# Optimization experiments

Measured on AMD Instinct MI355X. Metric: run time of the kernel, lower is better.

## Reference

```python
import jax, jax.numpy as jnp
import numpy as np


def reference(x, coef_ref, coef_qry):
    # x: [B, Hr, Wr, Hq, Wq] similarity tensor
    B, Hr, Wr, Hq, Wq = x.shape
    xr = x.reshape(B, Hr * Wr, Hq * Wq)  # [B, R, Q]
    # softmax over ref axis (axis=1) of coef_ref * (x - max over axis 1)
    xm_ref = xr - jnp.max(xr, axis=1, keepdims=True)
    conf_ref = jax.nn.softmax(coef_ref[0] * xm_ref, axis=1)
    # softmax over qry axis (axis=2) of coef_qry * (x - max over axis 2)
    xm_qry = xr - jnp.max(xr, axis=2, keepdims=True)
    conf_qry = jax.nn.softmax(coef_qry[0] * xm_qry, axis=2)
    confidence = jnp.sqrt(conf_ref * conf_qry)  # [B, R, Q]
    # top_k(k=1) over last axis + gather_nd of that value == max over axis 2
    values = jnp.max(confidence, axis=2)  # [B, R]
    return values.reshape(B, Hr, Wr, 1)


def setup_inputs() -> dict:
    key = jax.random.key(0)
    k1, = jax.random.split(key, 1)
    B, Hr, Wr, Hq, Wq = 16, 64, 64, 32, 32
    alpha = 10.0
    x = jax.random.normal(k1, (B, Hr, Wr, Hq, Wq), dtype=jnp.float32)
    coef_ref = jnp.full((1,), alpha, dtype=jnp.float32)
    coef_qry = jnp.full((1,), alpha, dtype=jnp.float32)
    return {"x": x, "coef_ref": coef_ref, "coef_qry": coef_qry}
```

## Files before the change

### kernel.cpp

```cpp
#include <hip/hip_runtime.h>
#include <math.h>
#include <stdint.h>


constexpr int B = 16;
constexpr int R = 4096;
constexpr int Q = 1024;
constexpr int CAP = 32;
constexpr int CHROWS = 16;
constexpr int NCH = R / CHROWS;
constexpr int NBLK = B * NCH;
#define DTH 1.1f
#define ECLAMP 80.f

__device__ __forceinline__ float wmax64(float v) {
#pragma unroll
    for (int o = 32; o; o >>= 1) v = fmaxf(v, __shfl_xor(v, o, 64));
    return v;
}
__device__ __forceinline__ float max4(float4 v) {
    return fmaxf(fmaxf(v.x, v.y), fmaxf(v.z, v.w));
}
__device__ __forceinline__ uint32_t encf(float f) {
    uint32_t u = __float_as_uint(f);
    return (u & 0x80000000u) ? ~u : (u | 0x80000000u);
}
__device__ __forceinline__ float decf(uint32_t e) {
    uint32_t u = (e & 0x80000000u) ? (e & 0x7FFFFFFFu) : ~e;
    return __uint_as_float(u);
}

__global__ __launch_bounds__(256, 8) void qatm_pass1(
    const float* __restrict__ x,
    float* __restrict__ psum,
    float2* __restrict__ rscnt,
    float4* __restrict__ cand4,
    uint32_t* __restrict__ candg,
    float* __restrict__ thChunk,
    uint32_t* __restrict__ cminEnc,
    const float* __restrict__ coef_ref,
    const float* __restrict__ coef_qry)
{
    const int blk = blockIdx.x;
    const int b = blk >> 8, ch = blk & (NCH - 1);
    const int t = threadIdx.x;
    const float ar = coef_ref[0], aq = coef_qry[0];
    const bool same = (ar == aq);

    __shared__ float ssum[CHROWS][257];
    __shared__ int cnt_sh[CHROWS];
    __shared__ float redsh[4];
    __shared__ float th_sh;

    if (blk < B && t == 0) cminEnc[blk] = 0xFFFFFFFFu;

    const size_t row0 = (size_t)b * R + (size_t)ch * CHROWS;
    const float4* xb = reinterpret_cast<const float4*>(x) + row0 * 256 + t;

    if (t < CHROWS) cnt_sh[t] = 0;
    {
        float m = wmax64(max4(xb[0]));
        if ((t & 63) == 0) redsh[t >> 6] = m;
        __syncthreads();
        if (t == 0) {
            float mm = fmaxf(fmaxf(redsh[0], redsh[1]), fmaxf(redsh[2], redsh[3]));
            th_sh = mm - DTH;
            thChunk[blk] = mm - DTH;
        }
        __syncthreads();
    }
    const float th = th_sh;

    float4 c = {0.f, 0.f, 0.f, 0.f};

#pragma unroll 4
    for (int r = 0; r < CHROWS; ++r) {
        float4 v = xb[(size_t)r * 256];
        float4 e;
        e.x = __expf(fminf(ar * v.x, ECLAMP));
        e.y = __expf(fminf(ar * v.y, ECLAMP));
        e.z = __expf(fminf(ar * v.z, ECLAMP));
        e.w = __expf(fminf(ar * v.w, ECLAMP));
        c.x += e.x; c.y += e.y; c.z += e.z; c.w += e.w;
        float rp;
        if (same) rp = (e.x + e.y) + (e.z + e.w);
        else rp = (__expf(fminf(aq * v.x, ECLAMP)) + __expf(fminf(aq * v.y, ECLAMP))) +
                  (__expf(fminf(aq * v.z, ECLAMP)) + __expf(fminf(aq * v.w, ECLAMP)));
        ssum[r][t] = rp;
        if (max4(v) >= th) {
            int idx = atomicAdd(&cnt_sh[r], 1);
            if (idx < CAP) {
                cand4[(row0 + r) * CAP + idx] = v;
                candg[(row0 + r) * CAP + idx] = (uint32_t)t;
            }
        }
    }

    __syncthreads();
    {
        const int row = t >> 4, seg = t & 15;
        float p = 0.f;
#pragma unroll
        for (int i = 0; i < 16; ++i) p += ssum[row][seg + 16 * i];
        p += __shfl_xor(p, 1, 64);
        p += __shfl_xor(p, 2, 64);
        p += __shfl_xor(p, 4, 64);
        p += __shfl_xor(p, 8, 64);
        if (seg == 0)
            rscnt[row0 + row] = make_float2(p, __uint_as_float((uint32_t)cnt_sh[row]));
    }
    reinterpret_cast<float4*>(psum)[(size_t)blk * 256 + t] = c;
}

__global__ __launch_bounds__(256) void qatm_combine(
    const float* __restrict__ psum, float* __restrict__ cvec,
    uint32_t* __restrict__ cminEnc)
{
    const int b = blockIdx.x >> 4, part = blockIdx.x & 15;
    const int t = threadIdx.x;
    const int col = part * 64 + (t & 63);
    const int stripe = t >> 6;
    __shared__ float acc[4][64];
    float s = 0.f;
    const float* p = psum + ((size_t)b * NCH + (size_t)stripe * 64) * 1024 + col;
#pragma unroll 8
    for (int i = 0; i < 64; ++i) s += p[(size_t)i * 1024];
    acc[stripe][t & 63] = s;
    __syncthreads();
    if (t < 64) {
        float tot = (acc[0][t] + acc[1][t]) + (acc[2][t] + acc[3][t]);
        float c = __logf(tot);
        cvec[b * 1024 + col] = c;
        float m = -wmax64(-c);
        if (t == 0) atomicMin(&cminEnc[b], encf(m));
    }
}

__global__ __launch_bounds__(256) void qatm_select(
    const float* __restrict__ x, const float* __restrict__ cvec,
    const uint32_t* __restrict__ cminEnc, const float* __restrict__ thChunk,
    const float2* __restrict__ rscnt,
    const float4* __restrict__ cand4, const uint32_t* __restrict__ candg,
    const float* __restrict__ coef_ref, const float* __restrict__ coef_qry,
    float* __restrict__ out)
{
    const int w = threadIdx.x >> 6, l = threadIdx.x & 63;
    const size_t row = (size_t)blockIdx.x * 4 + w;
    const int b = (int)(row >> 12);
    const float ar = coef_ref[0], aq = coef_qry[0], s2 = ar + aq;
    const float2 rc = rscnt[row];
    const float rs = rc.x;
    const uint32_t cnt = __float_as_uint(rc.y);

    float best = -INFINITY;
    bool fb = (cnt > CAP) || (cnt == 0) || !(s2 > 0.f);
    if (!fb) {
        if (l < (int)cnt) {
            float4 v = cand4[row * CAP + l];
            uint32_t g = candg[row * CAP + l];
            float4 c = reinterpret_cast<const float4*>(cvec)[((size_t)b << 8) + (int)(g & 255u)];
            best = fmaxf(fmaxf(s2 * v.x - c.x, s2 * v.y - c.y),
                         fmaxf(s2 * v.z - c.z, s2 * v.w - c.w));
        }
        best = wmax64(best);
        if (!(best >= s2 * thChunk[row >> 4] - decf(cminEnc[b]))) fb = true;
    }
    if (fb) {
        const float4* xr = reinterpret_cast<const float4*>(x) + row * (Q / 4);
        const float4* cq = reinterpret_cast<const float4*>(cvec) + ((size_t)b << 8);
        best = -INFINITY;
#pragma unroll
        for (int it = 0; it < 4; ++it) {
            float4 v = xr[it * 64 + l], c = cq[it * 64 + l];
            best = fmaxf(best, fmaxf(fmaxf(s2 * v.x - c.x, s2 * v.y - c.y),
                                     fmaxf(s2 * v.z - c.z, s2 * v.w - c.w)));
        }
        best = wmax64(best);
    }
    if (l == 0) out[row] = __expf(0.5f * (best - __logf(rs)));
}

extern "C" void kernel_launch(void* const* d_in, const int* in_sizes, int n_in,
                              void* d_out, int out_size, void* d_ws, size_t ws_size,
                              hipStream_t stream) {
    const float* x = (const float*)d_in[0];
    const float* coef_ref = (const float*)d_in[1];
    const float* coef_qry = (const float*)d_in[2];
    float* out = (float*)d_out;

    char* ws = (char*)d_ws;
    size_t off = 0;
    float4*   cand4 = (float4*)(ws + off);   off += (size_t)B * R * CAP * 16;
    uint32_t* candg = (uint32_t*)(ws + off); off += (size_t)B * R * CAP * 4;
    float*    psum  = (float*)(ws + off);    off += (size_t)NBLK * 1024 * 4;
    float*    cvec  = (float*)(ws + off);    off += (size_t)B * Q * 4;
    float2*   rscnt = (float2*)(ws + off);   off += (size_t)B * R * 8;
    float*    thA   = (float*)(ws + off);    off += (size_t)NBLK * 4;
    uint32_t* cminE = (uint32_t*)(ws + off); off += 64;

    qatm_pass1<<<NBLK, 256, 0, stream>>>(x, psum, rscnt, cand4, candg,
                                         thA, cminE, coef_ref, coef_qry);
    qatm_combine<<<256, 256, 0, stream>>>(psum, cvec, cminE);
    qatm_select<<<(B * R) / 4, 256, 0, stream>>>(x, cvec, cminE, thA, rscnt,
                                                 cand4, candg, coef_ref, coef_qry, out);
}
```

Baseline: 85.01 us.

## Store per-element candidates compactly in shared memory and batch select rows

Candidates are now recorded per scalar element as (value, column index) pairs, buffered in shared memory and written out coalesced at the end of the block, replacing scattered global writes of float4 plus group index. The main loop loads four rows at once with nontemporal loads to raise memory-level parallelism and avoid polluting cache. The select kernel handles four rows per wave, and the candidate cap drops to 16 elements, which shrinks workspace traffic. The cost is a higher chance of overflowing the cap and taking the full-row fallback, plus a serial atomic loop over set bits.

```diff
diff --git a/kernel.cpp b/kernel.cpp
--- a/kernel.cpp
+++ b/kernel.cpp
@@ -6,20 +6,19 @@
 constexpr int B = 16;
 constexpr int R = 4096;
 constexpr int Q = 1024;
-constexpr int CAP = 32;
+constexpr int CAPE = 16;
 constexpr int CHROWS = 16;
 constexpr int NCH = R / CHROWS;
 constexpr int NBLK = B * NCH;
 #define DTH 1.1f
 #define ECLAMP 80.f
 
+typedef float float4n __attribute__((ext_vector_type(4)));
+
 __device__ __forceinline__ float wmax64(float v) {
 #pragma unroll
     for (int o = 32; o; o >>= 1) v = fmaxf(v, __shfl_xor(v, o, 64));
     return v;
-}
-__device__ __forceinline__ float max4(float4 v) {
-    return fmaxf(fmaxf(v.x, v.y), fmaxf(v.z, v.w));
 }
 __device__ __forceinline__ uint32_t encf(float f) {
     uint32_t u = __float_as_uint(f);
@@ -34,8 +33,7 @@
     const float* __restrict__ x,
     float* __restrict__ psum,
     float2* __restrict__ rscnt,
-    float4* __restrict__ cand4,
-    uint32_t* __restrict__ candg,
+    float2* __restrict__ cand,
     float* __restrict__ thChunk,
     uint32_t* __restrict__ cminEnc,
     const float* __restrict__ coef_ref,
@@ -48,6 +46,7 @@
     const bool same = (ar == aq);
 
     __shared__ float ssum[CHROWS][257];
+    __shared__ float2 cand_sh[CHROWS][CAPE];
     __shared__ int cnt_sh[CHROWS];
     __shared__ float redsh[4];
     __shared__ float th_sh;
@@ -55,11 +54,12 @@
     if (blk < B && t == 0) cminEnc[blk] = 0xFFFFFFFFu;
 
     const size_t row0 = (size_t)b * R + (size_t)ch * CHROWS;
-    const float4* xb = reinterpret_cast<const float4*>(x) + row0 * 256 + t;
+    const float4n* xb = reinterpret_cast<const float4n*>(x) + row0 * 256 + t;
 
     if (t < CHROWS) cnt_sh[t] = 0;
     {
-        float m = wmax64(max4(xb[0]));
+        float4n s = xb[0];
+        float m = wmax64(fmaxf(fmaxf(s.x, s.y), fmaxf(s.z, s.w)));
         if ((t & 63) == 0) redsh[t >> 6] = m;
         __syncthreads();
         if (t == 0) {
@@ -73,25 +73,37 @@
 
     float4 c = {0.f, 0.f, 0.f, 0.f};
 
-#pragma unroll 4
-    for (int r = 0; r < CHROWS; ++r) {
-        float4 v = xb[(size_t)r * 256];
-        float4 e;
-        e.x = __expf(fminf(ar * v.x, ECLAMP));
-        e.y = __expf(fminf(ar * v.y, ECLAMP));
-        e.z = __expf(fminf(ar * v.z, ECLAMP));
-        e.w = __expf(fminf(ar * v.w, ECLAMP));
-        c.x += e.x; c.y += e.y; c.z += e.z; c.w += e.w;
-        float rp;
-        if (same) rp = (e.x + e.y) + (e.z + e.w);
-        else rp = (__expf(fminf(aq * v.x, ECLAMP)) + __expf(fminf(aq * v.y, ECLAMP))) +
-                  (__expf(fminf(aq * v.z, ECLAMP)) + __expf(fminf(aq * v.w, ECLAMP)));
-        ssum[r][t] = rp;
-        if (max4(v) >= th) {
-            int idx = atomicAdd(&cnt_sh[r], 1);
-            if (idx < CAP) {
-                cand4[(row0 + r) * CAP + idx] = v;
-                candg[(row0 + r) * CAP + idx] = (uint32_t)t;
+#pragma unroll
+    for (int r4 = 0; r4 < CHROWS; r4 += 4) {
+        float4n vn[4];
+#pragma unroll
+        for (int k = 0; k < 4; ++k)
+            vn[k] = __builtin_nontemporal_load(&xb[(size_t)(r4 + k) * 256]);
+#pragma unroll
+        for (int k = 0; k < 4; ++k) {
+            const int r = r4 + k;
+            const float vx = vn[k].x, vy = vn[k].y, vz = vn[k].z, vw = vn[k].w;
+            float ex = __expf(fminf(ar * vx, ECLAMP));
+            float ey = __expf(fminf(ar * vy, ECLAMP));
+            float ez = __expf(fminf(ar * vz, ECLAMP));
+            float ew = __expf(fminf(ar * vw, ECLAMP));
+            c.x += ex; c.y += ey; c.z += ez; c.w += ew;
+            float rp;
+            if (same) rp = (ex + ey) + (ez + ew);
+            else rp = (__expf(fminf(aq * vx, ECLAMP)) + __expf(fminf(aq * vy, ECLAMP))) +
+                      (__expf(fminf(aq * vz, ECLAMP)) + __expf(fminf(aq * vw, ECLAMP)));
+            ssum[r][t] = rp;
+            int m4 = (vx >= th ? 1 : 0) | (vy >= th ? 2 : 0) |
+                     (vz >= th ? 4 : 0) | (vw >= th ? 8 : 0);
+            if (m4) {
+                do {
+                    const int e = __ffs(m4) - 1;
+                    m4 &= m4 - 1;
+                    const float val = (e == 0) ? vx : (e == 1) ? vy : (e == 2) ? vz : vw;
+                    const int idx = atomicAdd(&cnt_sh[r], 1);
+                    if (idx < CAPE)
+                        cand_sh[r][idx] = make_float2(val, (float)(4 * t + e));
+                } while (m4);
             }
         }
     }
@@ -108,6 +120,9 @@
         p += __shfl_xor(p, 8, 64);
         if (seg == 0)
             rscnt[row0 + row] = make_float2(p, __uint_as_float((uint32_t)cnt_sh[row]));
+        const int cc = cnt_sh[row] < CAPE ? cnt_sh[row] : CAPE;
+        if (seg < cc)
+            cand[(row0 + row) * CAPE + seg] = cand_sh[row][seg];
     }
     reinterpret_cast<float4*>(psum)[(size_t)blk * 256 + t] = c;
 }
@@ -139,45 +154,45 @@
 __global__ __launch_bounds__(256) void qatm_select(
     const float* __restrict__ x, const float* __restrict__ cvec,
     const uint32_t* __restrict__ cminEnc, const float* __restrict__ thChunk,
-    const float2* __restrict__ rscnt,
-    const float4* __restrict__ cand4, const uint32_t* __restrict__ candg,
+    const float2* __restrict__ rscnt, const float2* __restrict__ cand,
     const float* __restrict__ coef_ref, const float* __restrict__ coef_qry,
     float* __restrict__ out)
 {
     const int w = threadIdx.x >> 6, l = threadIdx.x & 63;
-    const size_t row = (size_t)blockIdx.x * 4 + w;
-    const int b = (int)(row >> 12);
     const float ar = coef_ref[0], aq = coef_qry[0], s2 = ar + aq;
-    const float2 rc = rscnt[row];
-    const float rs = rc.x;
-    const uint32_t cnt = __float_as_uint(rc.y);
-
-    float best = -INFINITY;
-    bool fb = (cnt > CAP) || (cnt == 0) || !(s2 > 0.f);
-    if (!fb) {
-        if (l < (int)cnt) {
-            float4 v = cand4[row * CAP + l];
-            uint32_t g = candg[row * CAP + l];
-            float4 c = reinterpret_cast<const float4*>(cvec)[((size_t)b << 8) + (int)(g & 255u)];
-            best = fmaxf(fmaxf(s2 * v.x - c.x, s2 * v.y - c.y),
-                         fmaxf(s2 * v.z - c.z, s2 * v.w - c.w));
-        }
-        best = wmax64(best);
-        if (!(best >= s2 * thChunk[row >> 4] - decf(cminEnc[b]))) fb = true;
-    }
-    if (fb) {
-        const float4* xr = reinterpret_cast<const float4*>(x) + row * (Q / 4);
-        const float4* cq = reinterpret_cast<const float4*>(cvec) + ((size_t)b << 8);
-        best = -INFINITY;
-#pragma unroll
-        for (int it = 0; it < 4; ++it) {
-            float4 v = xr[it * 64 + l], c = cq[it * 64 + l];
-            best = fmaxf(best, fmaxf(fmaxf(s2 * v.x - c.x, s2 * v.y - c.y),
-                                     fmaxf(s2 * v.z - c.z, s2 * v.w - c.w)));
-        }
-        best = wmax64(best);
-    }
-    if (l == 0) out[row] = __expf(0.5f * (best - __logf(rs)));
+
+#pragma unroll
+    for (int i = 0; i < 4; ++i) {
+        const size_t row = (size_t)blockIdx.x * 16 + w * 4 + i;
+        const int b = (int)(row >> 12);
+        const float2 rc = rscnt[row];
+        const float rs = rc.x;
+        const uint32_t cnt = __float_as_uint(rc.y);
+
+        float best = -INFINITY;
+        bool fb = (cnt > CAPE) || (cnt == 0) || !(s2 > 0.f);
+        if (!fb) {
+            if (l < (int)cnt) {
+                float2 cd = cand[row * CAPE + l];
+                best = s2 * cd.x - cvec[((size_t)b << 10) + (int)cd.y];
+            }
+            best = wmax64(best);
+            if (!(best >= s2 * thChunk[row >> 4] - decf(cminEnc[b]))) fb = true;
+        }
+        if (fb) {
+            const float4* xr = reinterpret_cast<const float4*>(x) + row * (Q / 4);
+            const float4* cq = reinterpret_cast<const float4*>(cvec) + ((size_t)b << 8);
+            best = -INFINITY;
+#pragma unroll
+            for (int it = 0; it < 4; ++it) {
+                float4 v = xr[it * 64 + l], cc = cq[it * 64 + l];
+                best = fmaxf(best, fmaxf(fmaxf(s2 * v.x - cc.x, s2 * v.y - cc.y),
+                                         fmaxf(s2 * v.z - cc.z, s2 * v.w - cc.w)));
+            }
+            best = wmax64(best);
+        }
+        if (l == 0) out[row] = __expf(0.5f * (best - __logf(rs)));
+    }
 }
 
 extern "C" void kernel_launch(void* const* d_in, const int* in_sizes, int n_in,
@@ -190,17 +205,16 @@
 
     char* ws = (char*)d_ws;
     size_t off = 0;
-    float4*   cand4 = (float4*)(ws + off);   off += (size_t)B * R * CAP * 16;
-    uint32_t* candg = (uint32_t*)(ws + off); off += (size_t)B * R * CAP * 4;
+    float2*   cand  = (float2*)(ws + off);   off += (size_t)B * R * CAPE * 8;
     float*    psum  = (float*)(ws + off);    off += (size_t)NBLK * 1024 * 4;
     float*    cvec  = (float*)(ws + off);    off += (size_t)B * Q * 4;
     float2*   rscnt = (float2*)(ws + off);   off += (size_t)B * R * 8;
     float*    thA   = (float*)(ws + off);    off += (size_t)NBLK * 4;
     uint32_t* cminE = (uint32_t*)(ws + off); off += 64;
 
-    qatm_pass1<<<NBLK, 256, 0, stream>>>(x, psum, rscnt, cand4, candg,
+    qatm_pass1<<<NBLK, 256, 0, stream>>>(x, psum, rscnt, cand,
                                          thA, cminE, coef_ref, coef_qry);
     qatm_combine<<<256, 256, 0, stream>>>(psum, cvec, cminE);
-    qatm_select<<<(B * R) / 4, 256, 0, stream>>>(x, cvec, cminE, thA, rscnt,
-                                                 cand4, candg, coef_ref, coef_qry, out);
-}
+    qatm_select<<<(B * R) / 16, 256, 0, stream>>>(x, cvec, cminE, thA, rscnt,
+                                                  cand, coef_ref, coef_qry, out);
+}
```

Measured after the change: 126.5 us. +48.8%, slower.
